# Kernel tuning notes

Hardware: AMD Instinct MI355X
Metric: run time of the kernel (lower is better)

## Reference

```python
import jax, jax.numpy as jnp
import numpy as np

B, C, M, N = 16, 512, 256, 4096

def setup_inputs() -> dict:
    key = jax.random.key(0)
    k1, k2, k3 = jax.random.split(key, 3)
    x = jax.random.normal(k1, (B, C, N), dtype=jnp.float32)
    # Conv1d(C, M, 1, bias=False) weight: [M, C] (kernel size 1 squeezed)
    Wk = jax.random.normal(k2, (M, C), dtype=jnp.float32) * (1.0 / np.sqrt(C))
    # Conv1d(M, C, 1, bias=False) weight: [C, M]
    Wv = jax.random.normal(k3, (C, M), dtype=jnp.float32) * (1.0 / np.sqrt(M))
    return {"x": x, "Wk": Wk, "Wv": Wv}

def reference(x, Wk, Wv):
    # attn = M_k(x): 1x1 conv == matmul over channel dim -> [B, M, N]
    attn = jnp.einsum("mc,bcn->bmn", Wk, x)
    # softmax over sequence dim N
    attn = jax.nn.softmax(attn, axis=2)
    # L1 normalization over memory-unit (channel) dim M
    attn = attn / (1e-9 + attn.sum(axis=1, keepdims=True))
    # out = M_v(attn): [B, C, N]
    out = jnp.einsum("cm,bmn->bcn", Wv, attn)
    return x + out
```

## Files before the change

### kernel.cpp

```cpp
#include <hip/hip_runtime.h>
#include <hip/hip_bf16.h>

#define Bdim 16
#define Cdim 512
#define Mdim 256
#define Ndim 4096

typedef short bf16x8 __attribute__((ext_vector_type(8)));
typedef float f32x4 __attribute__((ext_vector_type(4)));
typedef unsigned short us8 __attribute__((ext_vector_type(8)));
typedef unsigned short us4 __attribute__((ext_vector_type(4)));

__device__ __forceinline__ unsigned short f2b(float f) {
  union { float f; unsigned int u; } v; v.f = f;
  return (unsigned short)((v.u + 0x8000u) >> 16);
}
__device__ __forceinline__ float b2f(unsigned short h) {
  union { unsigned int u; float f; } v; v.u = ((unsigned int)h) << 16;
  return v.f;
}

__global__ __launch_bounds__(256) void k0_convert(
    const float* __restrict__ gWk, const float* __restrict__ gWv,
    unsigned short* __restrict__ oWk, unsigned short* __restrict__ oWv) {
  const int i = (blockIdx.x * 256 + threadIdx.x) * 4;
  f32x4 a = *reinterpret_cast<const f32x4*>(gWk + i);
  f32x4 b = *reinterpret_cast<const f32x4*>(gWv + i);
  us4 ha, hb;
#pragma unroll
  for (int j = 0; j < 4; ++j) { ha[j] = f2b(a[j]); hb[j] = f2b(b[j]); }
  *reinterpret_cast<us4*>(oWk + i) = ha;
  *reinterpret_cast<us4*>(oWv + i) = hb;
}

#define K1_XPAD 72

__global__ __launch_bounds__(256) void k1_gemm1(
    const float* __restrict__ gx, const unsigned short* __restrict__ gWkB,
    unsigned short* __restrict__ gS) {
  __shared__ unsigned short Wk_s[128 * 64];
  __shared__ unsigned short xT_s[128 * K1_XPAD];
  const int t = threadIdx.x;
  const int b = blockIdx.z;
  const int m0 = blockIdx.y * 128;
  const int n0 = blockIdx.x * 128;
  const int w = t >> 6;
  const int lane = t & 63;
  const int lr = lane & 15;
  const int lg = lane >> 4;
  const int wm = (w >> 1) * 64;
  const int wn = (w & 1) * 64;

  f32x4 acc[4][4] = {};
  const float* xb = gx + (size_t)b * Cdim * Ndim + n0;

  const int snl = t & 63;
  const int scb = (t >> 6) * 16;
  const int wrow = lane >> 3;
  const int wchk = (lane & 7) ^ (wrow & 7);

  for (int ck = 0; ck < Cdim; ck += 64) {
    {
      const unsigned short* gsrc =
          gWkB + (size_t)(m0 + w * 32 + wrow) * Cdim + ck + wchk * 8;
#pragma unroll
      for (int j = 0; j < 4; ++j) {
        __builtin_amdgcn_global_load_lds(
            (const __attribute__((address_space(1))) unsigned int*)(gsrc + (size_t)j * 8 * Cdim),
            (__attribute__((address_space(3))) unsigned int*)&Wk_s[(w * 32 + j * 8) * 64],
            16, 0, 0);
      }
    }
#pragma unroll
    for (int h = 0; h < 2; ++h) {
      const int n = snl + h * 64;
      const float* src = xb + (size_t)(ck + scb) * Ndim + n;
      float xv[16];
#pragma unroll
      for (int j = 0; j < 16; ++j) xv[j] = src[(size_t)j * Ndim];
      us8 h0, h1;
#pragma unroll
      for (int j = 0; j < 8; ++j) {
        h0[j] = (unsigned short)(__float_as_uint(xv[j]) >> 16);
        h1[j] = (unsigned short)(__float_as_uint(xv[8 + j]) >> 16);
      }
      *reinterpret_cast<us8*>(&xT_s[n * K1_XPAD + scb]) = h0;
      *reinterpret_cast<us8*>(&xT_s[n * K1_XPAD + scb + 8]) = h1;
    }
    __syncthreads();
#pragma unroll
    for (int kk = 0; kk < 64; kk += 32) {
      bf16x8 af[4], bfr[4];
#pragma unroll
      for (int mi = 0; mi < 4; ++mi) {
        const int rm = wm + mi * 16 + lr;
        af[mi] = *reinterpret_cast<const bf16x8*>(
            reinterpret_cast<const char*>(Wk_s) +
            rm * 128 + ((kk * 2 + lg * 16) ^ ((rm & 7) << 4)));
      }
#pragma unroll
      for (int ni = 0; ni < 4; ++ni)
        bfr[ni] = *reinterpret_cast<const bf16x8*>(
            &xT_s[(wn + ni * 16 + lr) * K1_XPAD + kk + lg * 8]);
#pragma unroll
      for (int mi = 0; mi < 4; ++mi)
#pragma unroll
        for (int ni = 0; ni < 4; ++ni)
          acc[mi][ni] = __builtin_amdgcn_mfma_f32_16x16x32_bf16(
              af[mi], bfr[ni], acc[mi][ni], 0, 0, 0);
    }
    __syncthreads();
  }
  unsigned short* Sb = gS + ((size_t)b * Mdim + m0 + wm) * Ndim + n0 + wn;
#pragma unroll
  for (int mi = 0; mi < 4; ++mi)
#pragma unroll
    for (int ni = 0; ni < 4; ++ni)
#pragma unroll
      for (int r = 0; r < 4; ++r) {
        int m = mi * 16 + lg * 4 + r;
        int n = ni * 16 + lr;
        Sb[(size_t)m * Ndim + n] = f2b(acc[mi][ni][r]);
      }
}

__global__ __launch_bounds__(256) void k2_rowstats(
    const unsigned short* __restrict__ gS, float* __restrict__ stats) {
  const int m = blockIdx.x;
  const int b = blockIdx.y;
  const unsigned short* row = gS + ((size_t)b * Mdim + m) * Ndim;
  const int t = threadIdx.x;
  const int w = t >> 6;
  float s = 0.f;
#pragma unroll
  for (int i = 0; i < 2; ++i) {
    us8 u = *reinterpret_cast<const us8*>(row + i * 2048 + t * 8);
#pragma unroll
    for (int j = 0; j < 8; ++j) s += __expf(b2f(u[j]));
  }
#pragma unroll
  for (int o = 32; o > 0; o >>= 1) s += __shfl_xor(s, o, 64);
  __shared__ float redsum[4];
  if ((t & 63) == 0) redsum[w] = s;
  __syncthreads();
  if (t == 0) {
    float tot = redsum[0] + redsum[1] + redsum[2] + redsum[3];
    stats[(size_t)b * Mdim + m] = 1.0f / tot;
  }
}

#define K3_PAD 264

__global__ __launch_bounds__(256) void k3_norm(
    const unsigned short* __restrict__ gS, const float* __restrict__ stats,
    unsigned short* __restrict__ gPT) {
  __shared__ unsigned short P_s[64 * K3_PAD];
  __shared__ float cs[4][64];
  __shared__ float rtot[64];
  const int b = blockIdx.y;
  const int n0 = blockIdx.x * 64;
  const int t = threadIdx.x;
  const int w = t >> 6;
  const int l = t & 63;
  const unsigned short* Sb = gS + ((size_t)b * Mdim + w * 64) * Ndim + n0 + l;
  const float* stb = stats + (size_t)b * Mdim + w * 64;
  float acc = 0.f;
#pragma unroll
  for (int i8 = 0; i8 < 8; ++i8) {
    us8 pk;
#pragma unroll
    for (int jj = 0; jj < 8; ++jj) {
      const int mi = i8 * 8 + jj;
      float p = __expf(b2f(Sb[(size_t)mi * Ndim])) * stb[mi];
      acc += p;
      pk[jj] = f2b(p);
    }
    *reinterpret_cast<us8*>(&P_s[l * K3_PAD + w * 64 + i8 * 8]) = pk;
  }
  cs[w][l] = acc;
  __syncthreads();
  if (w == 0) rtot[l] = 1.0f / (1e-9f + cs[0][l] + cs[1][l] + cs[2][l] + cs[3][l]);
  __syncthreads();
  const int mo = (t & 31) * 8;
#pragma unroll
  for (int j = 0; j < 8; ++j) {
    const int n = (t >> 5) + j * 8;
    const float rc = rtot[n];
    us8 pv = *reinterpret_cast<const us8*>(&P_s[n * K3_PAD + mo]);
    us8 o;
#pragma unroll
    for (int q = 0; q < 8; ++q) o[q] = f2b(b2f(pv[q]) * rc);
    *reinterpret_cast<us8*>(gPT + ((size_t)b * Ndim + n0 + n) * Mdim + mo) = o;
  }
}

#define K4_P 136

__global__ __launch_bounds__(256) void k4_gemm2(
    const float* __restrict__ gx, const unsigned short* __restrict__ gWvB,
    const unsigned short* __restrict__ gPT, float* __restrict__ gout) {
  __shared__ unsigned short Wv_s[128 * K4_P];
  __shared__ unsigned short PT_s[64 * K4_P];
  const int t = threadIdx.x;
  const int b = blockIdx.z;
  const int c0 = blockIdx.y * 128;
  const int n0 = blockIdx.x * 64;
  const int w = t >> 6;
  const int lane = t & 63;
  const int lr = lane & 15;
  const int lg = lane >> 4;
  const int wc = (w >> 1) * 64;
  const int wn = (w & 1) * 32;

  f32x4 acc[4][2] = {};

  for (int ck = 0; ck < Mdim; ck += 128) {
#pragma unroll
    for (int i = 0; i < 8; ++i) {
      int q = i * 256 + t;
      int r = q >> 4;
      int mq = (q & 15) * 8;
      us8 u = *reinterpret_cast<const us8*>(gWvB + (size_t)(c0 + r) * Mdim + ck + mq);
      *reinterpret_cast<us8*>(&Wv_s[r * K4_P + mq]) = u;
    }
#pragma unroll
    for (int i = 0; i < 4; ++i) {
      int q = i * 256 + t;
      int r = q >> 4;
      int mq = (q & 15) * 8;
      us8 u = *reinterpret_cast<const us8*>(gPT + ((size_t)b * Ndim + n0 + r) * Mdim + ck + mq);
      *reinterpret_cast<us8*>(&PT_s[r * K4_P + mq]) = u;
    }
    __syncthreads();
#pragma unroll
    for (int kk = 0; kk < 128; kk += 32) {
      bf16x8 af[4], bfr[2];
#pragma unroll
      for (int ci = 0; ci < 4; ++ci)
        af[ci] = *reinterpret_cast<const bf16x8*>(
            &Wv_s[(wc + ci * 16 + lr) * K4_P + kk + lg * 8]);
#pragma unroll
      for (int ni = 0; ni < 2; ++ni)
        bfr[ni] = *reinterpret_cast<const bf16x8*>(
            &PT_s[(wn + ni * 16 + lr) * K4_P + kk + lg * 8]);
#pragma unroll
      for (int ci = 0; ci < 4; ++ci)
#pragma unroll
        for (int ni = 0; ni < 2; ++ni)
          acc[ci][ni] = __builtin_amdgcn_mfma_f32_16x16x32_bf16(
              af[ci], bfr[ni], acc[ci][ni], 0, 0, 0);
    }
    __syncthreads();
  }
#pragma unroll
  for (int ci = 0; ci < 4; ++ci)
#pragma unroll
    for (int ni = 0; ni < 2; ++ni)
#pragma unroll
      for (int r = 0; r < 4; ++r) {
        int c = c0 + wc + ci * 16 + lg * 4 + r;
        int n = n0 + wn + ni * 16 + lr;
        size_t idx = ((size_t)b * Cdim + c) * Ndim + n;
        gout[idx] = gx[idx] + acc[ci][ni][r];
      }
}

extern "C" void kernel_launch(void* const* d_in, const int* in_sizes, int n_in,
                              void* d_out, int out_size, void* d_ws, size_t ws_size,
                              hipStream_t stream) {
  const float* x = (const float*)d_in[0];
  const float* Wk = (const float*)d_in[1];
  const float* Wv = (const float*)d_in[2];
  float* out = (float*)d_out;

  unsigned short* S = (unsigned short*)d_ws;
  unsigned short* PT = S + (size_t)Bdim * Mdim * Ndim;
  float* stats = (float*)(PT + (size_t)Bdim * Ndim * Mdim);
  unsigned short* WkB = (unsigned short*)(stats + Bdim * Mdim);
  unsigned short* WvB = WkB + Mdim * Cdim;

  k0_convert<<<dim3((Mdim * Cdim) / 1024), 256, 0, stream>>>(Wk, Wv, WkB, WvB);
  k1_gemm1<<<dim3(Ndim / 128, Mdim / 128, Bdim), 256, 0, stream>>>(x, WkB, S);
  k2_rowstats<<<dim3(Mdim, Bdim), 256, 0, stream>>>(S, stats);
  k3_norm<<<dim3(Ndim / 64, Bdim), 256, 0, stream>>>(S, stats, PT);
  k4_gemm2<<<dim3(Ndim / 64, Cdim / 128, Bdim), 256, 0, stream>>>(x, WvB, PT, out);
}
```

Measured before the change: 124.0 us.

## Fuse softmax row-sum partials into GEMM1 epilogue and prefetch GEMM2 second K-chunk

The exp-sum for each row is now computed in the GEMM1 epilogue from the rounded bf16 values and written as per-block partial sums. A tiny reduce kernel combines them, which removes the separate pass that re-read the full S matrix. GEMM2's K loop is manually unrolled into two chunks, and the second chunk's global loads are issued before the first chunk's MFMAs so the load latency overlaps with compute. The cost is more registers in GEMM2 and an extra partial-sum buffer in the workspace.

```diff
diff --git a/kernel.cpp b/kernel.cpp
--- a/kernel.cpp
+++ b/kernel.cpp
@@ -37,9 +37,10 @@
 
 __global__ __launch_bounds__(256) void k1_gemm1(
     const float* __restrict__ gx, const unsigned short* __restrict__ gWkB,
-    unsigned short* __restrict__ gS) {
+    unsigned short* __restrict__ gS, float* __restrict__ gPsum) {
   __shared__ unsigned short Wk_s[128 * 64];
   __shared__ unsigned short xT_s[128 * K1_XPAD];
+  __shared__ float rsum2[2][128];
   const int t = threadIdx.x;
   const int b = blockIdx.z;
   const int m0 = blockIdx.y * 128;
@@ -115,38 +116,35 @@
 #pragma unroll
   for (int mi = 0; mi < 4; ++mi)
 #pragma unroll
-    for (int ni = 0; ni < 4; ++ni)
-#pragma unroll
-      for (int r = 0; r < 4; ++r) {
-        int m = mi * 16 + lg * 4 + r;
-        int n = ni * 16 + lr;
-        Sb[(size_t)m * Ndim + n] = f2b(acc[mi][ni][r]);
-      }
-}
-
-__global__ __launch_bounds__(256) void k2_rowstats(
-    const unsigned short* __restrict__ gS, float* __restrict__ stats) {
-  const int m = blockIdx.x;
-  const int b = blockIdx.y;
-  const unsigned short* row = gS + ((size_t)b * Mdim + m) * Ndim;
-  const int t = threadIdx.x;
-  const int w = t >> 6;
+    for (int r = 0; r < 4; ++r) {
+      float s = 0.f;
+#pragma unroll
+      for (int ni = 0; ni < 4; ++ni) {
+        const unsigned short h = f2b(acc[mi][ni][r]);
+        const int m = mi * 16 + lg * 4 + r;
+        const int n = ni * 16 + lr;
+        Sb[(size_t)m * Ndim + n] = h;
+        s += __expf(b2f(h));
+      }
+#pragma unroll
+      for (int o = 1; o < 16; o <<= 1) s += __shfl_xor(s, o, 64);
+      if (lr == 0) rsum2[w & 1][wm + mi * 16 + lg * 4 + r] = s;
+    }
+  __syncthreads();
+  if (t < 128)
+    gPsum[((size_t)b * 32 + blockIdx.x) * Mdim + m0 + t] =
+        rsum2[0][t] + rsum2[1][t];
+}
+
+__global__ __launch_bounds__(256) void k2_reduce(
+    const float* __restrict__ gPsum, float* __restrict__ stats) {
+  const int b = blockIdx.x;
+  const int m = threadIdx.x;
   float s = 0.f;
 #pragma unroll
-  for (int i = 0; i < 2; ++i) {
-    us8 u = *reinterpret_cast<const us8*>(row + i * 2048 + t * 8);
-#pragma unroll
-    for (int j = 0; j < 8; ++j) s += __expf(b2f(u[j]));
-  }
-#pragma unroll
-  for (int o = 32; o > 0; o >>= 1) s += __shfl_xor(s, o, 64);
-  __shared__ float redsum[4];
-  if ((t & 63) == 0) redsum[w] = s;
-  __syncthreads();
-  if (t == 0) {
-    float tot = redsum[0] + redsum[1] + redsum[2] + redsum[3];
-    stats[(size_t)b * Mdim + m] = 1.0f / tot;
-  }
+  for (int nb = 0; nb < 32; ++nb)
+    s += gPsum[((size_t)b * 32 + nb) * Mdim + m];
+  stats[b * Mdim + m] = 1.0f / s;
 }
 
 #define K3_PAD 264
@@ -212,46 +210,85 @@
   const int wc = (w >> 1) * 64;
   const int wn = (w & 1) * 32;
 
+  const int sr = t >> 4;
+  const int smq = (t & 15) * 8;
+
   f32x4 acc[4][2] = {};
 
-  for (int ck = 0; ck < Mdim; ck += 128) {
-#pragma unroll
-    for (int i = 0; i < 8; ++i) {
-      int q = i * 256 + t;
-      int r = q >> 4;
-      int mq = (q & 15) * 8;
-      us8 u = *reinterpret_cast<const us8*>(gWvB + (size_t)(c0 + r) * Mdim + ck + mq);
-      *reinterpret_cast<us8*>(&Wv_s[r * K4_P + mq]) = u;
-    }
-#pragma unroll
-    for (int i = 0; i < 4; ++i) {
-      int q = i * 256 + t;
-      int r = q >> 4;
-      int mq = (q & 15) * 8;
-      us8 u = *reinterpret_cast<const us8*>(gPT + ((size_t)b * Ndim + n0 + r) * Mdim + ck + mq);
-      *reinterpret_cast<us8*>(&PT_s[r * K4_P + mq]) = u;
-    }
-    __syncthreads();
-#pragma unroll
-    for (int kk = 0; kk < 128; kk += 32) {
-      bf16x8 af[4], bfr[2];
-#pragma unroll
-      for (int ci = 0; ci < 4; ++ci)
-        af[ci] = *reinterpret_cast<const bf16x8*>(
-            &Wv_s[(wc + ci * 16 + lr) * K4_P + kk + lg * 8]);
+  us8 wv_r[8], pt_r[4];
+#pragma unroll
+  for (int i = 0; i < 8; ++i)
+    wv_r[i] = *reinterpret_cast<const us8*>(
+        gWvB + (size_t)(c0 + i * 16 + sr) * Mdim + smq);
+#pragma unroll
+  for (int i = 0; i < 4; ++i)
+    pt_r[i] = *reinterpret_cast<const us8*>(
+        gPT + ((size_t)b * Ndim + n0 + i * 16 + sr) * Mdim + smq);
+#pragma unroll
+  for (int i = 0; i < 8; ++i)
+    *reinterpret_cast<us8*>(&Wv_s[(i * 16 + sr) * K4_P + smq]) = wv_r[i];
+#pragma unroll
+  for (int i = 0; i < 4; ++i)
+    *reinterpret_cast<us8*>(&PT_s[(i * 16 + sr) * K4_P + smq]) = pt_r[i];
+  __syncthreads();
+
+  us8 wv2_r[8], pt2_r[4];
+#pragma unroll
+  for (int i = 0; i < 8; ++i)
+    wv2_r[i] = *reinterpret_cast<const us8*>(
+        gWvB + (size_t)(c0 + i * 16 + sr) * Mdim + 128 + smq);
+#pragma unroll
+  for (int i = 0; i < 4; ++i)
+    pt2_r[i] = *reinterpret_cast<const us8*>(
+        gPT + ((size_t)b * Ndim + n0 + i * 16 + sr) * Mdim + 128 + smq);
+
+#pragma unroll
+  for (int kk = 0; kk < 128; kk += 32) {
+    bf16x8 af[4], bfr[2];
+#pragma unroll
+    for (int ci = 0; ci < 4; ++ci)
+      af[ci] = *reinterpret_cast<const bf16x8*>(
+          &Wv_s[(wc + ci * 16 + lr) * K4_P + kk + lg * 8]);
+#pragma unroll
+    for (int ni = 0; ni < 2; ++ni)
+      bfr[ni] = *reinterpret_cast<const bf16x8*>(
+          &PT_s[(wn + ni * 16 + lr) * K4_P + kk + lg * 8]);
+#pragma unroll
+    for (int ci = 0; ci < 4; ++ci)
 #pragma unroll
       for (int ni = 0; ni < 2; ++ni)
-        bfr[ni] = *reinterpret_cast<const bf16x8*>(
-            &PT_s[(wn + ni * 16 + lr) * K4_P + kk + lg * 8]);
-#pragma unroll
-      for (int ci = 0; ci < 4; ++ci)
-#pragma unroll
-        for (int ni = 0; ni < 2; ++ni)
-          acc[ci][ni] = __builtin_amdgcn_mfma_f32_16x16x32_bf16(
-              af[ci], bfr[ni], acc[ci][ni], 0, 0, 0);
-    }
-    __syncthreads();
-  }
+        acc[ci][ni] = __builtin_amdgcn_mfma_f32_16x16x32_bf16(
+            af[ci], bfr[ni], acc[ci][ni], 0, 0, 0);
+  }
+  __syncthreads();
+
+#pragma unroll
+  for (int i = 0; i < 8; ++i)
+    *reinterpret_cast<us8*>(&Wv_s[(i * 16 + sr) * K4_P + smq]) = wv2_r[i];
+#pragma unroll
+  for (int i = 0; i < 4; ++i)
+    *reinterpret_cast<us8*>(&PT_s[(i * 16 + sr) * K4_P + smq]) = pt2_r[i];
+  __syncthreads();
+
+#pragma unroll
+  for (int kk = 0; kk < 128; kk += 32) {
+    bf16x8 af[4], bfr[2];
+#pragma unroll
+    for (int ci = 0; ci < 4; ++ci)
+      af[ci] = *reinterpret_cast<const bf16x8*>(
+          &Wv_s[(wc + ci * 16 + lr) * K4_P + kk + lg * 8]);
+#pragma unroll
+    for (int ni = 0; ni < 2; ++ni)
+      bfr[ni] = *reinterpret_cast<const bf16x8*>(
+          &PT_s[(wn + ni * 16 + lr) * K4_P + kk + lg * 8]);
+#pragma unroll
+    for (int ci = 0; ci < 4; ++ci)
+#pragma unroll
+      for (int ni = 0; ni < 2; ++ni)
+        acc[ci][ni] = __builtin_amdgcn_mfma_f32_16x16x32_bf16(
+            af[ci], bfr[ni], acc[ci][ni], 0, 0, 0);
+  }
+
 #pragma unroll
   for (int ci = 0; ci < 4; ++ci)
 #pragma unroll
@@ -276,12 +313,13 @@
   unsigned short* S = (unsigned short*)d_ws;
   unsigned short* PT = S + (size_t)Bdim * Mdim * Ndim;
   float* stats = (float*)(PT + (size_t)Bdim * Ndim * Mdim);
-  unsigned short* WkB = (unsigned short*)(stats + Bdim * Mdim);
+  float* psum = stats + Bdim * Mdim;
+  unsigned short* WkB = (unsigned short*)(psum + Bdim * 32 * Mdim);
   unsigned short* WvB = WkB + Mdim * Cdim;
 
   k0_convert<<<dim3((Mdim * Cdim) / 1024), 256, 0, stream>>>(Wk, Wv, WkB, WvB);
-  k1_gemm1<<<dim3(Ndim / 128, Mdim / 128, Bdim), 256, 0, stream>>>(x, WkB, S);
-  k2_rowstats<<<dim3(Mdim, Bdim), 256, 0, stream>>>(S, stats);
+  k1_gemm1<<<dim3(Ndim / 128, Mdim / 128, Bdim), 256, 0, stream>>>(x, WkB, S, psum);
+  k2_reduce<<<dim3(Bdim), 256, 0, stream>>>(psum, stats);
   k3_norm<<<dim3(Ndim / 64, Bdim), 256, 0, stream>>>(S, stats, PT);
   k4_gemm2<<<dim3(Ndim / 64, Cdim / 128, Bdim), 256, 0, stream>>>(x, WvB, PT, out);
 }
```

Measured after the change: 127.6 us. 2.9% more time.
